# Kernel optimization log

Measured on AMD Instinct MI355X. Metric: run time of the kernel, lower is better.

The kernel has to match this reference:

```python
import jax, jax.numpy as jnp
import numpy as np

H = 8        # num_heads
D = 64       # qkv_dim
E = 512      # embed_dim = H*D
MS = 16      # ms_hidden_dim


def setup_inputs() -> dict:
    key = jax.random.key(0)
    ks = jax.random.split(key, 12)
    b, r, c = 4, 512, 512
    row_emb = jax.random.normal(ks[0], (b, r, E), dtype=jnp.float32)
    col_emb = jax.random.normal(ks[1], (b, c, E), dtype=jnp.float32)
    cost_mat = jax.random.uniform(ks[2], (b, r, c), dtype=jnp.float32)
    attn_mask = jax.random.randint(ks[3], (b, H, r, c), 0, 2) > 0
    s = 1.0 / np.sqrt(E)
    Wq = jax.random.uniform(ks[4], (H * D, E), minval=-s, maxval=s)
    Wk = jax.random.uniform(ks[5], (H * D, E), minval=-s, maxval=s)
    Wv = jax.random.uniform(ks[6], (H * D, E), minval=-s, maxval=s)
    Wout = jax.random.uniform(ks[7], (E, E), minval=-s, maxval=s)
    m1 = np.sqrt(0.5)
    m2 = np.sqrt(1.0 / MS)
    Wmix1 = jax.random.uniform(ks[8], (H * MS, 2 * H), minval=-m1, maxval=m1)
    Wmix2 = jax.random.uniform(ks[9], (H, H * MS), minval=-m2, maxval=m2)
    return {"row_emb": row_emb, "col_emb": col_emb, "cost_mat": cost_mat,
            "attn_mask": attn_mask, "Wq": Wq, "Wk": Wk, "Wv": Wv,
            "Wmix1": Wmix1, "Wmix2": Wmix2, "Wout": Wout}


def reference(row_emb, col_emb, cost_mat, attn_mask, Wq, Wk, Wv, Wmix1, Wmix2, Wout):
    b, r, _ = row_emb.shape
    c = col_emb.shape[1]
    norm = 1.0 / jnp.sqrt(jnp.asarray(D, row_emb.dtype))
    # projections -> [b, h, s, d]
    q = (row_emb @ Wq.T).reshape(b, r, H, D).transpose(0, 2, 1, 3)
    k = (col_emb @ Wk.T).reshape(b, c, H, D).transpose(0, 2, 1, 3)
    v = (col_emb @ Wv.T).reshape(b, c, H, D).transpose(0, 2, 1, 3)
    dot = norm * jnp.einsum('bhrd,bhcd->bhrc', q, k)            # [b,h,r,c]
    cost = jnp.broadcast_to(cost_mat[:, None, :, :], dot.shape)  # [b,h,r,c]
    # stack then rearrange 'b h r c s -> b r c (h s)' (h major, s minor)
    two = jnp.stack([dot, cost], axis=-1)                        # [b,h,r,c,2]
    two = two.transpose(0, 2, 3, 1, 4).reshape(b, r, c, 2 * H)
    hid = jax.nn.relu(two @ Wmix1.T)                             # [b,r,c,H*MS]
    ms = hid @ Wmix2.T                                           # [b,r,c,H]
    logits = ms.transpose(0, 3, 1, 2)                            # [b,h,r,c]
    # mask handling: rows that are fully masked become fully unmasked
    all_masked = jnp.all(attn_mask, axis=-1, keepdims=True)
    mask = jnp.where(all_masked, False, attn_mask)
    logits = jnp.where(mask, -jnp.inf, logits)
    weights = jax.nn.softmax(logits, axis=-1)
    out = jnp.einsum('bhrc,bhcd->bhrd', weights, v)              # [b,h,r,d]
    out = out.transpose(0, 2, 1, 3).reshape(b, r, H * D)         # b s (h d)
    return out @ Wout.T
```

## Files before the change

kernel.cpp:

```cpp
#include <hip/hip_runtime.h>
#include <math.h>

typedef __attribute__((ext_vector_type(8))) short bf16x8;
typedef __attribute__((ext_vector_type(4))) float f32x4;
typedef unsigned short ushort_t;

static __device__ inline unsigned short f2bf(float f) {
    union { float f; unsigned u; } v; v.f = f;
    unsigned r = v.u + 0x7fff + ((v.u >> 16) & 1);
    return (unsigned short)(r >> 16);
}

#if defined(__has_builtin)
#  if __has_builtin(__builtin_amdgcn_cvt_pk_bf16_f32)
#    define HAVE_PK_BF16 1
#  endif
#endif

static __device__ inline unsigned pk2bf(float a, float b) {
#ifdef HAVE_PK_BF16
    auto r = __builtin_amdgcn_cvt_pk_bf16_f32(a, b);
    unsigned u; __builtin_memcpy(&u, &r, 4);
    return u;
#else
    return (unsigned)f2bf(a) | ((unsigned)f2bf(b) << 16);
#endif
}

__global__ __launch_bounds__(256) void convert_all(const float* __restrict__ a0,
                                                   const float* __restrict__ a1,
                                                   const float* __restrict__ a2,
                                                   const float* __restrict__ a3,
                                                   const float* __restrict__ a4,
                                                   const float* __restrict__ a5,
                                                   ushort_t* __restrict__ dst) {
    const size_t e = ((size_t)blockIdx.x * 256 + threadIdx.x) * 4;
    const float* src; size_t off;
    if      (e < 1048576) { src = a0; off = 0; }
    else if (e < 2097152) { src = a1; off = 1048576; }
    else if (e < 2359296) { src = a2; off = 2097152; }
    else if (e < 2621440) { src = a3; off = 2359296; }
    else if (e < 2883584) { src = a4; off = 2621440; }
    else                  { src = a5; off = 2883584; }
    const float4 v = *(const float4*)(src + (e - off));
    uint2 o; o.x = pk2bf(v.x, v.y); o.y = pk2bf(v.z, v.w);
    *(uint2*)(dst + e) = o;
}

template<int OM>
__global__ __launch_bounds__(256) void gemm_bt(const ushort_t* __restrict__ A,
                                               const ushort_t* __restrict__ B,
                                               void* __restrict__ C) {
    const int t    = threadIdx.x;
    const int w    = t >> 6;
    const int lane = t & 63;
    const int quad = lane >> 4;
    const int sl   = lane & 15;
    const int m0 = blockIdx.x * 64 + (w >> 1) * 32;
    const int n0 = blockIdx.y * 64 + (w & 1) * 32;

    f32x4 acc[2][2] = {};

    for (int k0 = 0; k0 < 512; k0 += 32) {
        bf16x8 a[2], b[2];
#pragma unroll
        for (int rs = 0; rs < 2; ++rs)
            a[rs] = *(const bf16x8*)(A + (size_t)(m0 + rs * 16 + sl) * 512 + k0 + quad * 8);
#pragma unroll
        for (int cs = 0; cs < 2; ++cs)
            b[cs] = *(const bf16x8*)(B + (size_t)(n0 + cs * 16 + sl) * 512 + k0 + quad * 8);
#pragma unroll
        for (int rs = 0; rs < 2; ++rs)
#pragma unroll
            for (int cs = 0; cs < 2; ++cs)
                acc[rs][cs] = __builtin_amdgcn_mfma_f32_16x16x32_bf16(a[rs], b[cs], acc[rs][cs], 0, 0, 0);
    }

#pragma unroll
    for (int rs = 0; rs < 2; ++rs)
#pragma unroll
        for (int cs = 0; cs < 2; ++cs) {
            const int n = n0 + cs * 16 + sl;
            if (OM == 2) {
                const int mb   = m0 + rs * 16 + quad * 4;
                const int bidx = mb >> 9, c = mb & 511;
                const int h = n >> 6, d = n & 63;
                ushort4 o;
                o.x = f2bf(acc[rs][cs][0]); o.y = f2bf(acc[rs][cs][1]);
                o.z = f2bf(acc[rs][cs][2]); o.w = f2bf(acc[rs][cs][3]);
                *(ushort4*)((ushort_t*)C + (size_t)(((bidx * 8 + h) * 64 + d)) * 512 + c) = o;
            } else {
#pragma unroll
                for (int reg = 0; reg < 4; ++reg) {
                    const int m = m0 + rs * 16 + quad * 4 + reg;
                    if (OM == 0)
                        ((ushort_t*)C)[(size_t)m * 512 + n] = f2bf(acc[rs][cs][reg]);
                    else
                        ((float*)C)[(size_t)m * 512 + n] = acc[rs][cs][reg];
                }
            }
        }
}

__global__ __launch_bounds__(256) void pv_bt(const ushort_t* __restrict__ P,
                                             const ushort_t* __restrict__ Vt,
                                             ushort_t* __restrict__ Aout) {
    const int t    = threadIdx.x;
    const int w    = t >> 6;
    const int lane = t & 63;
    const int quad = lane >> 4;
    const int sl   = lane & 15;
    const int bh = blockIdx.y;
    const int m0 = blockIdx.x * 64 + (w >> 1) * 32;
    const int n0 = (w & 1) * 32;

    const ushort_t* A = P  + (size_t)bh * 512 * 512;
    const ushort_t* B = Vt + (size_t)bh * 64 * 512;
    ushort_t* Cb = Aout + (size_t)(bh >> 3) * 512 * 512 + (bh & 7) * 64;

    f32x4 acc[2][2] = {};

    for (int k0 = 0; k0 < 512; k0 += 32) {
        bf16x8 a[2], b[2];
#pragma unroll
        for (int rs = 0; rs < 2; ++rs)
            a[rs] = *(const bf16x8*)(A + (size_t)(m0 + rs * 16 + sl) * 512 + k0 + quad * 8);
#pragma unroll
        for (int cs = 0; cs < 2; ++cs)
            b[cs] = *(const bf16x8*)(B + (size_t)(n0 + cs * 16 + sl) * 512 + k0 + quad * 8);
#pragma unroll
        for (int rs = 0; rs < 2; ++rs)
#pragma unroll
            for (int cs = 0; cs < 2; ++cs)
                acc[rs][cs] = __builtin_amdgcn_mfma_f32_16x16x32_bf16(a[rs], b[cs], acc[rs][cs], 0, 0, 0);
    }

#pragma unroll
    for (int rs = 0; rs < 2; ++rs)
#pragma unroll
        for (int cs = 0; cs < 2; ++cs) {
            const int n = n0 + cs * 16 + sl;
#pragma unroll
            for (int reg = 0; reg < 4; ++reg) {
                const int m = m0 + rs * 16 + quad * 4 + reg;
                Cb[(size_t)m * 512 + n] = f2bf(acc[rs][cs][reg]);
            }
        }
}

__global__ __launch_bounds__(256) void dot_mlp_v3(const ushort_t* __restrict__ Qb,
                                                  const ushort_t* __restrict__ Kb,
                                                  const float* __restrict__ cost,
                                                  const float* __restrict__ W1,
                                                  const float* __restrict__ W2,
                                                  float* __restrict__ logits) {
    __shared__ ushort_t Xs[1024 * 18];
    __shared__ ushort_t hidS[4 * 16 * 136];
    __shared__ ushort_t W1fs[128 * 16];
    __shared__ ushort_t W2ss[8 * 128];

    const int b  = blockIdx.z;
    const int r0 = blockIdx.y * 32;
    const int c0 = blockIdx.x * 32;
    const int t    = threadIdx.x;
    const int w    = t >> 6;
    const int lane = t & 63;
    const int quad = lane >> 4;
    const int sl   = lane & 15;

    const bf16x8 zf = {0, 0, 0, 0, 0, 0, 0, 0};

    {
        int4 z = {0, 0, 0, 0};
#pragma unroll
        for (int i = 0; i < 9; ++i) ((int4*)Xs)[t + i * 256] = z;
    }
    if (t < 128) {
        float s = 0.f;
#pragma unroll
        for (int h = 0; h < 8; ++h) {
            W1fs[t * 16 + h] = f2bf(W1[t * 16 + 2 * h]);
            s += W1[t * 16 + 2 * h + 1];
        }
        W1fs[t * 16 + 8] = f2bf(s);
#pragma unroll
        for (int k = 9; k < 16; ++k) W1fs[t * 16 + k] = 0;
    }
#pragma unroll
    for (int i = 0; i < 4; ++i) {
        const int idx = t + i * 256;
        W2ss[idx] = f2bf(W2[idx]);
    }
    __syncthreads();

#pragma unroll
    for (int i = 0; i < 4; ++i) {
        const int cell = t + i * 256;
        const int rl = cell >> 5, cl = cell & 31;
        Xs[cell * 18 + 8] = f2bf(cost[((size_t)b * 512 + r0 + rl) * 512 + c0 + cl]);
    }

    f32x4 dacc[2][2][2];
#pragma unroll
    for (int hh = 0; hh < 2; ++hh) {
        const int h = 2 * w + hh;
        bf16x8 af[2][2], bfr[2][2];
#pragma unroll
        for (int rs = 0; rs < 2; ++rs)
#pragma unroll
            for (int ks = 0; ks < 2; ++ks)
                af[rs][ks] = *(const bf16x8*)(Qb +
                    ((size_t)(b * 512 + r0 + rs * 16 + sl) * 512 + h * 64 + ks * 32 + quad * 8));
#pragma unroll
        for (int cs = 0; cs < 2; ++cs)
#pragma unroll
            for (int ks = 0; ks < 2; ++ks)
                bfr[cs][ks] = *(const bf16x8*)(Kb +
                    ((size_t)(b * 512 + c0 + cs * 16 + sl) * 512 + h * 64 + ks * 32 + quad * 8));
#pragma unroll
        for (int rs = 0; rs < 2; ++rs)
#pragma unroll
            for (int cs = 0; cs < 2; ++cs) {
                f32x4 acc = {0.f, 0.f, 0.f, 0.f};
                acc = __builtin_amdgcn_mfma_f32_16x16x32_bf16(af[rs][0], bfr[cs][0], acc, 0, 0, 0);
                acc = __builtin_amdgcn_mfma_f32_16x16x32_bf16(af[rs][1], bfr[cs][1], acc, 0, 0, 0);
                dacc[hh][rs][cs] = acc;
            }
    }
#pragma unroll
    for (int rs = 0; rs < 2; ++rs)
#pragma unroll
        for (int cs = 0; cs < 2; ++cs)
#pragma unroll
            for (int reg = 0; reg < 4; ++reg) {
                const int cell = (rs * 16 + quad * 4 + reg) * 32 + cs * 16 + sl;
                ((unsigned*)Xs)[cell * 9 + w] =
                    pk2bf(dacc[0][rs][cs][reg] * 0.125f, dacc[1][rs][cs][reg] * 0.125f);
            }

    __syncthreads();

    bf16x8 bw1[8];
#pragma unroll
    for (int nt = 0; nt < 8; ++nt)
        bw1[nt] = (quad < 2) ? *(const bf16x8*)&W1fs[(nt * 16 + sl) * 16 + quad * 8] : zf;
    bf16x8 bw2[4];
#pragma unroll
    for (int ks = 0; ks < 4; ++ks)
        bw2[ks] = (sl < 8) ? *(const bf16x8*)&W2ss[sl * 128 + ks * 32 + quad * 8] : zf;

    ushort_t* hidW = hidS + w * (16 * 136);

    for (int mt = 0; mt < 16; ++mt) {
        const int gmt = w * 16 + mt;
        const int cb  = gmt * 16;

        bf16x8 a1 = zf;
        if (quad < 2) {
            const unsigned* xr = (const unsigned*)Xs + (size_t)(cb + sl) * 9 + quad * 4;
            union { unsigned u[4]; bf16x8 v; } tmp;
            tmp.u[0] = xr[0]; tmp.u[1] = xr[1]; tmp.u[2] = xr[2]; tmp.u[3] = xr[3];
            a1 = tmp.v;
        }
        f32x4 hacc[8];
#pragma unroll
        for (int nt = 0; nt < 8; ++nt) {
            f32x4 z = {0.f, 0.f, 0.f, 0.f};
            hacc[nt] = __builtin_amdgcn_mfma_f32_16x16x32_bf16(a1, bw1[nt], z, 0, 0, 0);
        }
#pragma unroll
        for (int nt = 0; nt < 8; ++nt)
#pragma unroll
            for (int rp = 0; rp < 4; rp += 2) {
                const unsigned u = pk2bf(fmaxf(hacc[nt][rp], 0.f), fmaxf(hacc[nt][rp + 1], 0.f));
                hidW[(quad * 4 + rp) * 136 + nt * 16 + sl]     = (ushort_t)u;
                hidW[(quad * 4 + rp + 1) * 136 + nt * 16 + sl] = (ushort_t)(u >> 16);
            }

        f32x4 acc2 = {0.f, 0.f, 0.f, 0.f};
#pragma unroll
        for (int ks = 0; ks < 4; ++ks) {
            const ushort_t* hp = hidW + sl * 136 + ks * 32 + quad * 8;
            union { unsigned u[4]; bf16x8 v; } tu;
            *(uint2*)&tu.u[0] = *(const uint2*)hp;
            *(uint2*)&tu.u[2] = *(const uint2*)(hp + 4);
            acc2 = __builtin_amdgcn_mfma_f32_16x16x32_bf16(tu.v, bw2[ks], acc2, 0, 0, 0);
        }

        if (sl < 8) {
            const int r = r0 + (gmt >> 1);
            const int cbase = c0 + (gmt & 1) * 16 + quad * 4;
            float4 o; o.x = acc2[0]; o.y = acc2[1]; o.z = acc2[2]; o.w = acc2[3];
            *(float4*)&logits[((size_t)(b * 8 + sl) * 512 + r) * 512 + cbase] = o;
        }
    }
}

__global__ __launch_bounds__(256) void softmax_mask(const float* __restrict__ logits,
                                                    const int* __restrict__ mask,
                                                    ushort_t* __restrict__ Pb) {
    const int wave = threadIdx.x / 64;
    const int lane = threadIdx.x % 64;
    const size_t rowIdx = (size_t)blockIdx.x * 4 + wave;
    const float* lp = logits + rowIdx * 512;
    const int* mp = mask + rowIdx * 512;

    float v[8];
    int   m[8];
    int allm = 1;
#pragma unroll
    for (int i = 0; i < 8; ++i) {
        v[i] = lp[lane + i * 64];
        m[i] = mp[lane + i * 64];
        allm &= (m[i] != 0);
    }
    const bool all_masked = (__all(allm) != 0);

    float mx = -__builtin_inff();
#pragma unroll
    for (int i = 0; i < 8; ++i) {
        const bool keep = all_masked || (m[i] == 0);
        if (keep) mx = fmaxf(mx, v[i]);
    }
#pragma unroll
    for (int s = 32; s > 0; s >>= 1) mx = fmaxf(mx, __shfl_xor(mx, s, 64));

    float e[8];
    float sum = 0.f;
#pragma unroll
    for (int i = 0; i < 8; ++i) {
        const bool keep = all_masked || (m[i] == 0);
        e[i] = keep ? __expf(v[i] - mx) : 0.f;
        sum += e[i];
    }
#pragma unroll
    for (int s = 32; s > 0; s >>= 1) sum += __shfl_xor(sum, s, 64);

    const float inv = 1.f / sum;
#pragma unroll
    for (int i = 0; i < 8; ++i)
        Pb[rowIdx * 512 + lane + i * 64] = f2bf(e[i] * inv);
}

extern "C" void kernel_launch(void* const* d_in, const int* in_sizes, int n_in,
                              void* d_out, int out_size, void* d_ws, size_t ws_size,
                              hipStream_t stream) {
    const float* row_emb = (const float*)d_in[0];
    const float* col_emb = (const float*)d_in[1];
    const float* cost    = (const float*)d_in[2];
    const int*   mask    = (const int*)d_in[3];
    const float* Wq      = (const float*)d_in[4];
    const float* Wk      = (const float*)d_in[5];
    const float* Wv      = (const float*)d_in[6];
    const float* Wmix1   = (const float*)d_in[7];
    const float* Wmix2   = (const float*)d_in[8];
    const float* Wout    = (const float*)d_in[9];
    float* out = (float*)d_out;

    char* ws = (char*)d_ws;
    const size_t MB = (size_t)1 << 20;
    ushort_t* convDst = (ushort_t*)ws;
    ushort_t* rowb  = (ushort_t*)(ws);
    ushort_t* colb  = (ushort_t*)(ws + 2 * MB);
    ushort_t* Wqb   = (ushort_t*)(ws + 4 * MB);
    ushort_t* Wkb   = (ushort_t*)(ws + 4 * MB + 512 * 1024);
    ushort_t* Wvb   = (ushort_t*)(ws + 5 * MB);
    ushort_t* Woutb = (ushort_t*)(ws + 5 * MB + 512 * 1024);
    ushort_t* Qb    = (ushort_t*)(ws + 6 * MB);
    ushort_t* Kb    = (ushort_t*)(ws + 8 * MB);
    ushort_t* Vt    = (ushort_t*)(ws + 10 * MB);
    ushort_t* Aoutb = (ushort_t*)(ws + 12 * MB);
    ushort_t* Pb    = (ushort_t*)(ws + 16 * MB);
    float* logitsBuf = (float*)(ws + 40 * MB);

    convert_all<<<3072, 256, 0, stream>>>(row_emb, col_emb, Wq, Wk, Wv, Wout, convDst);

    dim3 g1(32, 8);
    gemm_bt<0><<<g1, 256, 0, stream>>>(rowb, Wqb, Qb);
    gemm_bt<0><<<g1, 256, 0, stream>>>(colb, Wkb, Kb);
    gemm_bt<2><<<g1, 256, 0, stream>>>(colb, Wvb, Vt);

    dim3 g2(16, 16, 4);
    dot_mlp_v3<<<g2, 256, 0, stream>>>(Qb, Kb, cost, Wmix1, Wmix2, logitsBuf);

    softmax_mask<<<4096, 256, 0, stream>>>(logitsBuf, mask, Pb);

    pv_bt<<<dim3(8, 32), 256, 0, stream>>>(Pb, Vt, Aoutb);

    gemm_bt<1><<<g1, 256, 0, stream>>>(Aoutb, Woutb, out);
}
```

Baseline: 194.9 us.

## Batch QKV GEMMs, fuse softmax with PV, widen dot-MLP kernel to 512 threads

The three Q/K/V projection GEMMs become one launch indexed by blockIdx.z. Softmax and the P·V product are fused so the probabilities stay in shared memory and the bf16 P buffer round-trip through global memory is gone. The dot/MLP kernel moves to 512 threads with one head per wave. It also interleaves the hidden-layer MFMAs with the second-layer MFMA in small chunks, which shrinks the shared hidden buffer and drops the separate zero-fill pass. In exchange, the fused PV kernel issues less MFMA work per block, and the new W2 fragment permutation has to line up with the packed hidden layout.

```diff
diff --git a/kernel.cpp b/kernel.cpp
--- a/kernel.cpp
+++ b/kernel.cpp
@@ -47,10 +47,18 @@
     *(uint2*)(dst + e) = o;
 }
 
-template<int OM>
-__global__ __launch_bounds__(256) void gemm_bt(const ushort_t* __restrict__ A,
-                                               const ushort_t* __restrict__ B,
-                                               void* __restrict__ C) {
+__global__ __launch_bounds__(256) void gemm_qkv(const ushort_t* __restrict__ rowb,
+                                                const ushort_t* __restrict__ colb,
+                                                const ushort_t* __restrict__ Wqb,
+                                                const ushort_t* __restrict__ Wkb,
+                                                const ushort_t* __restrict__ Wvb,
+                                                ushort_t* __restrict__ Qb,
+                                                ushort_t* __restrict__ Kb,
+                                                ushort_t* __restrict__ Vt) {
+    const int z = blockIdx.z;
+    const ushort_t* A = (z == 0) ? rowb : colb;
+    const ushort_t* B = (z == 0) ? Wqb : (z == 1) ? Wkb : Wvb;
+
     const int t    = threadIdx.x;
     const int w    = t >> 6;
     const int lane = t & 63;
@@ -81,42 +89,35 @@
 #pragma unroll
         for (int cs = 0; cs < 2; ++cs) {
             const int n = n0 + cs * 16 + sl;
-            if (OM == 2) {
+            if (z == 2) {
                 const int mb   = m0 + rs * 16 + quad * 4;
                 const int bidx = mb >> 9, c = mb & 511;
                 const int h = n >> 6, d = n & 63;
                 ushort4 o;
                 o.x = f2bf(acc[rs][cs][0]); o.y = f2bf(acc[rs][cs][1]);
                 o.z = f2bf(acc[rs][cs][2]); o.w = f2bf(acc[rs][cs][3]);
-                *(ushort4*)((ushort_t*)C + (size_t)(((bidx * 8 + h) * 64 + d)) * 512 + c) = o;
+                *(ushort4*)(Vt + (size_t)(((bidx * 8 + h) * 64 + d)) * 512 + c) = o;
             } else {
+                ushort_t* C = (z == 0) ? Qb : Kb;
 #pragma unroll
                 for (int reg = 0; reg < 4; ++reg) {
                     const int m = m0 + rs * 16 + quad * 4 + reg;
-                    if (OM == 0)
-                        ((ushort_t*)C)[(size_t)m * 512 + n] = f2bf(acc[rs][cs][reg]);
-                    else
-                        ((float*)C)[(size_t)m * 512 + n] = acc[rs][cs][reg];
+                    C[(size_t)m * 512 + n] = f2bf(acc[rs][cs][reg]);
                 }
             }
         }
 }
 
-__global__ __launch_bounds__(256) void pv_bt(const ushort_t* __restrict__ P,
-                                             const ushort_t* __restrict__ Vt,
-                                             ushort_t* __restrict__ Aout) {
+__global__ __launch_bounds__(256) void gemm_out(const ushort_t* __restrict__ A,
+                                                const ushort_t* __restrict__ B,
+                                                float* __restrict__ C) {
     const int t    = threadIdx.x;
     const int w    = t >> 6;
     const int lane = t & 63;
     const int quad = lane >> 4;
     const int sl   = lane & 15;
-    const int bh = blockIdx.y;
     const int m0 = blockIdx.x * 64 + (w >> 1) * 32;
-    const int n0 = (w & 1) * 32;
-
-    const ushort_t* A = P  + (size_t)bh * 512 * 512;
-    const ushort_t* B = Vt + (size_t)bh * 64 * 512;
-    ushort_t* Cb = Aout + (size_t)(bh >> 3) * 512 * 512 + (bh & 7) * 64;
+    const int n0 = blockIdx.y * 64 + (w & 1) * 32;
 
     f32x4 acc[2][2] = {};
 
@@ -143,19 +144,19 @@
 #pragma unroll
             for (int reg = 0; reg < 4; ++reg) {
                 const int m = m0 + rs * 16 + quad * 4 + reg;
-                Cb[(size_t)m * 512 + n] = f2bf(acc[rs][cs][reg]);
+                C[(size_t)m * 512 + n] = acc[rs][cs][reg];
             }
         }
 }
 
-__global__ __launch_bounds__(256) void dot_mlp_v3(const ushort_t* __restrict__ Qb,
+__global__ __launch_bounds__(512) void dot_mlp_v4(const ushort_t* __restrict__ Qb,
                                                   const ushort_t* __restrict__ Kb,
                                                   const float* __restrict__ cost,
                                                   const float* __restrict__ W1,
                                                   const float* __restrict__ W2,
                                                   float* __restrict__ logits) {
     __shared__ ushort_t Xs[1024 * 18];
-    __shared__ ushort_t hidS[4 * 16 * 136];
+    __shared__ ushort_t hidS[8 * 16 * 36];
     __shared__ ushort_t W1fs[128 * 16];
     __shared__ ushort_t W2ss[8 * 128];
 
@@ -170,11 +171,6 @@
 
     const bf16x8 zf = {0, 0, 0, 0, 0, 0, 0, 0};
 
-    {
-        int4 z = {0, 0, 0, 0};
-#pragma unroll
-        for (int i = 0; i < 9; ++i) ((int4*)Xs)[t + i * 256] = z;
-    }
     if (t < 128) {
         float s = 0.f;
 #pragma unroll
@@ -187,23 +183,19 @@
         for (int k = 9; k < 16; ++k) W1fs[t * 16 + k] = 0;
     }
 #pragma unroll
-    for (int i = 0; i < 4; ++i) {
-        const int idx = t + i * 256;
-        W2ss[idx] = f2bf(W2[idx]);
-    }
-    __syncthreads();
-
-#pragma unroll
-    for (int i = 0; i < 4; ++i) {
-        const int cell = t + i * 256;
+    for (int i = 0; i < 2; ++i) W2ss[t + i * 512] = f2bf(W2[t + i * 512]);
+
+#pragma unroll
+    for (int i = 0; i < 2; ++i) {
+        const int cell = t + i * 512;
         const int rl = cell >> 5, cl = cell & 31;
-        Xs[cell * 18 + 8] = f2bf(cost[((size_t)b * 512 + r0 + rl) * 512 + c0 + cl]);
-    }
-
-    f32x4 dacc[2][2][2];
-#pragma unroll
-    for (int hh = 0; hh < 2; ++hh) {
-        const int h = 2 * w + hh;
+        unsigned* base = (unsigned*)(Xs + cell * 18 + 8);
+        base[0] = (unsigned)f2bf(cost[((size_t)b * 512 + r0 + rl) * 512 + c0 + cl]);
+        base[1] = 0; base[2] = 0; base[3] = 0; base[4] = 0;
+    }
+
+    {
+        const int h = w;
         bf16x8 af[2][2], bfr[2][2];
 #pragma unroll
         for (int rs = 0; rs < 2; ++rs)
@@ -224,19 +216,13 @@
                 f32x4 acc = {0.f, 0.f, 0.f, 0.f};
                 acc = __builtin_amdgcn_mfma_f32_16x16x32_bf16(af[rs][0], bfr[cs][0], acc, 0, 0, 0);
                 acc = __builtin_amdgcn_mfma_f32_16x16x32_bf16(af[rs][1], bfr[cs][1], acc, 0, 0, 0);
-                dacc[hh][rs][cs] = acc;
+#pragma unroll
+                for (int reg = 0; reg < 4; ++reg) {
+                    const int cell = (rs * 16 + quad * 4 + reg) * 32 + cs * 16 + sl;
+                    Xs[cell * 18 + h] = f2bf(acc[reg] * 0.125f);
+                }
             }
     }
-#pragma unroll
-    for (int rs = 0; rs < 2; ++rs)
-#pragma unroll
-        for (int cs = 0; cs < 2; ++cs)
-#pragma unroll
-            for (int reg = 0; reg < 4; ++reg) {
-                const int cell = (rs * 16 + quad * 4 + reg) * 32 + cs * 16 + sl;
-                ((unsigned*)Xs)[cell * 9 + w] =
-                    pk2bf(dacc[0][rs][cs][reg] * 0.125f, dacc[1][rs][cs][reg] * 0.125f);
-            }
 
     __syncthreads();
 
@@ -246,13 +232,22 @@
         bw1[nt] = (quad < 2) ? *(const bf16x8*)&W1fs[(nt * 16 + sl) * 16 + quad * 8] : zf;
     bf16x8 bw2[4];
 #pragma unroll
-    for (int ks = 0; ks < 4; ++ks)
-        bw2[ks] = (sl < 8) ? *(const bf16x8*)&W2ss[sl * 128 + ks * 32 + quad * 8] : zf;
-
-    ushort_t* hidW = hidS + w * (16 * 136);
-
-    for (int mt = 0; mt < 16; ++mt) {
-        const int gmt = w * 16 + mt;
+    for (int ks = 0; ks < 4; ++ks) {
+        union { ushort_t s[8]; bf16x8 v; } tu;
+#pragma unroll
+        for (int i = 0; i < 8; ++i) {
+            const int p  = quad * 8 + i;
+            const int jc = (p >> 1) | ((p & 1) << 4);
+            tu.s[i] = (sl < 8) ? W2ss[sl * 128 + ks * 32 + jc] : (ushort_t)0;
+        }
+        bw2[ks] = tu.v;
+    }
+
+    ushort_t* hidW = hidS + w * (16 * 36);
+
+#pragma unroll
+    for (int mt = 0; mt < 8; ++mt) {
+        const int gmt = w * 8 + mt;
         const int cb  = gmt * 16;
 
         bf16x8 a1 = zf;
@@ -262,28 +257,21 @@
             tmp.u[0] = xr[0]; tmp.u[1] = xr[1]; tmp.u[2] = xr[2]; tmp.u[3] = xr[3];
             a1 = tmp.v;
         }
-        f32x4 hacc[8];
-#pragma unroll
-        for (int nt = 0; nt < 8; ++nt) {
+
+        f32x4 acc2 = {0.f, 0.f, 0.f, 0.f};
+#pragma unroll
+        for (int ks = 0; ks < 4; ++ks) {
             f32x4 z = {0.f, 0.f, 0.f, 0.f};
-            hacc[nt] = __builtin_amdgcn_mfma_f32_16x16x32_bf16(a1, bw1[nt], z, 0, 0, 0);
-        }
-#pragma unroll
-        for (int nt = 0; nt < 8; ++nt)
-#pragma unroll
-            for (int rp = 0; rp < 4; rp += 2) {
-                const unsigned u = pk2bf(fmaxf(hacc[nt][rp], 0.f), fmaxf(hacc[nt][rp + 1], 0.f));
-                hidW[(quad * 4 + rp) * 136 + nt * 16 + sl]     = (ushort_t)u;
-                hidW[(quad * 4 + rp + 1) * 136 + nt * 16 + sl] = (ushort_t)(u >> 16);
-            }
-
-        f32x4 acc2 = {0.f, 0.f, 0.f, 0.f};
-#pragma unroll
-        for (int ks = 0; ks < 4; ++ks) {
-            const ushort_t* hp = hidW + sl * 136 + ks * 32 + quad * 8;
-            union { unsigned u[4]; bf16x8 v; } tu;
-            *(uint2*)&tu.u[0] = *(const uint2*)hp;
-            *(uint2*)&tu.u[2] = *(const uint2*)(hp + 4);
+            const f32x4 h0 = __builtin_amdgcn_mfma_f32_16x16x32_bf16(a1, bw1[2 * ks],     z, 0, 0, 0);
+            const f32x4 h1 = __builtin_amdgcn_mfma_f32_16x16x32_bf16(a1, bw1[2 * ks + 1], z, 0, 0, 0);
+#pragma unroll
+            for (int rp = 0; rp < 4; ++rp)
+                ((unsigned*)hidW)[(quad * 4 + rp) * 18 + sl] =
+                    pk2bf(fmaxf(h0[rp], 0.f), fmaxf(h1[rp], 0.f));
+            union { uint2 u2[2]; bf16x8 v; } tu;
+            const ushort_t* hp = hidW + sl * 36 + quad * 8;
+            tu.u2[0] = *(const uint2*)hp;
+            tu.u2[1] = *(const uint2*)(hp + 4);
             acc2 = __builtin_amdgcn_mfma_f32_16x16x32_bf16(tu.v, bw2[ks], acc2, 0, 0, 0);
         }
 
@@ -296,50 +284,93 @@
     }
 }
 
-__global__ __launch_bounds__(256) void softmax_mask(const float* __restrict__ logits,
-                                                    const int* __restrict__ mask,
-                                                    ushort_t* __restrict__ Pb) {
-    const int wave = threadIdx.x / 64;
-    const int lane = threadIdx.x % 64;
-    const size_t rowIdx = (size_t)blockIdx.x * 4 + wave;
-    const float* lp = logits + rowIdx * 512;
-    const int* mp = mask + rowIdx * 512;
-
-    float v[8];
-    int   m[8];
-    int allm = 1;
-#pragma unroll
-    for (int i = 0; i < 8; ++i) {
-        v[i] = lp[lane + i * 64];
-        m[i] = mp[lane + i * 64];
-        allm &= (m[i] != 0);
-    }
-    const bool all_masked = (__all(allm) != 0);
-
-    float mx = -__builtin_inff();
-#pragma unroll
-    for (int i = 0; i < 8; ++i) {
-        const bool keep = all_masked || (m[i] == 0);
-        if (keep) mx = fmaxf(mx, v[i]);
-    }
-#pragma unroll
-    for (int s = 32; s > 0; s >>= 1) mx = fmaxf(mx, __shfl_xor(mx, s, 64));
-
-    float e[8];
-    float sum = 0.f;
-#pragma unroll
-    for (int i = 0; i < 8; ++i) {
-        const bool keep = all_masked || (m[i] == 0);
-        e[i] = keep ? __expf(v[i] - mx) : 0.f;
-        sum += e[i];
-    }
-#pragma unroll
-    for (int s = 32; s > 0; s >>= 1) sum += __shfl_xor(sum, s, 64);
-
-    const float inv = 1.f / sum;
-#pragma unroll
-    for (int i = 0; i < 8; ++i)
-        Pb[rowIdx * 512 + lane + i * 64] = f2bf(e[i] * inv);
+__global__ __launch_bounds__(256) void softmax_pv(const float* __restrict__ logits,
+                                                  const int* __restrict__ mask,
+                                                  const ushort_t* __restrict__ Vt,
+                                                  ushort_t* __restrict__ Aout) {
+    __shared__ ushort_t Ps[32 * 520];
+
+    const int t    = threadIdx.x;
+    const int w    = t >> 6;
+    const int lane = t & 63;
+    const int quad = lane >> 4;
+    const int sl   = lane & 15;
+    const int rt = blockIdx.x;
+    const int bh = blockIdx.y;
+    const int r0 = rt * 32;
+
+#pragma unroll
+    for (int rr = 0; rr < 8; ++rr) {
+        const int row = w * 8 + rr;
+        const float* lp = logits + ((size_t)bh * 512 + r0 + row) * 512;
+        const int*   mp = mask   + ((size_t)bh * 512 + r0 + row) * 512;
+
+        float v[8]; int m[8]; int allm = 1;
+#pragma unroll
+        for (int i = 0; i < 8; ++i) {
+            v[i] = lp[lane + i * 64];
+            m[i] = mp[lane + i * 64];
+            allm &= (m[i] != 0);
+        }
+        const bool all_masked = (__all(allm) != 0);
+
+        float mx = -__builtin_inff();
+#pragma unroll
+        for (int i = 0; i < 8; ++i) {
+            const bool keep = all_masked || (m[i] == 0);
+            if (keep) mx = fmaxf(mx, v[i]);
+        }
+#pragma unroll
+        for (int s = 32; s > 0; s >>= 1) mx = fmaxf(mx, __shfl_xor(mx, s, 64));
+
+        float e[8]; float sum = 0.f;
+#pragma unroll
+        for (int i = 0; i < 8; ++i) {
+            const bool keep = all_masked || (m[i] == 0);
+            e[i] = keep ? __expf(v[i] - mx) : 0.f;
+            sum += e[i];
+        }
+#pragma unroll
+        for (int s = 32; s > 0; s >>= 1) sum += __shfl_xor(sum, s, 64);
+
+        const float inv = 1.f / sum;
+#pragma unroll
+        for (int i = 0; i < 8; ++i)
+            Ps[row * 520 + lane + i * 64] = f2bf(e[i] * inv);
+    }
+
+    __syncthreads();
+
+    const int mt  = w >> 1;
+    const int n0w = (w & 1) * 32;
+    const ushort_t* vb = Vt + (size_t)bh * 64 * 512;
+
+    f32x4 acc[2] = {};
+    for (int ks = 0; ks < 16; ++ks) {
+        union { uint2 u2[2]; bf16x8 v; } ta;
+        const ushort_t* pp = Ps + (size_t)(mt * 16 + sl) * 520 + ks * 32 + quad * 8;
+        ta.u2[0] = *(const uint2*)pp;
+        ta.u2[1] = *(const uint2*)(pp + 4);
+        bf16x8 bv[2];
+#pragma unroll
+        for (int cn = 0; cn < 2; ++cn)
+            bv[cn] = *(const bf16x8*)(vb + (size_t)(n0w + cn * 16 + sl) * 512 + ks * 32 + quad * 8);
+#pragma unroll
+        for (int cn = 0; cn < 2; ++cn)
+            acc[cn] = __builtin_amdgcn_mfma_f32_16x16x32_bf16(ta.v, bv[cn], acc[cn], 0, 0, 0);
+    }
+
+    const int bidx = bh >> 3, h = bh & 7;
+    ushort_t* Cb = Aout + (size_t)bidx * 512 * 512 + h * 64;
+#pragma unroll
+    for (int cn = 0; cn < 2; ++cn) {
+        const int n = n0w + cn * 16 + sl;
+#pragma unroll
+        for (int reg = 0; reg < 4; ++reg) {
+            const int m = r0 + mt * 16 + quad * 4 + reg;
+            Cb[(size_t)m * 512 + n] = f2bf(acc[cn][reg]);
+        }
+    }
 }
 
 extern "C" void kernel_launch(void* const* d_in, const int* in_sizes, int n_in,
@@ -370,22 +401,15 @@
     ushort_t* Kb    = (ushort_t*)(ws + 8 * MB);
     ushort_t* Vt    = (ushort_t*)(ws + 10 * MB);
     ushort_t* Aoutb = (ushort_t*)(ws + 12 * MB);
-    ushort_t* Pb    = (ushort_t*)(ws + 16 * MB);
     float* logitsBuf = (float*)(ws + 40 * MB);
 
     convert_all<<<3072, 256, 0, stream>>>(row_emb, col_emb, Wq, Wk, Wv, Wout, convDst);
 
-    dim3 g1(32, 8);
-    gemm_bt<0><<<g1, 256, 0, stream>>>(rowb, Wqb, Qb);
-    gemm_bt<0><<<g1, 256, 0, stream>>>(colb, Wkb, Kb);
-    gemm_bt<2><<<g1, 256, 0, stream>>>(colb, Wvb, Vt);
-
-    dim3 g2(16, 16, 4);
-    dot_mlp_v3<<<g2, 256, 0, stream>>>(Qb, Kb, cost, Wmix1, Wmix2, logitsBuf);
-
-    softmax_mask<<<4096, 256, 0, stream>>>(logitsBuf, mask, Pb);
-
-    pv_bt<<<dim3(8, 32), 256, 0, stream>>>(Pb, Vt, Aoutb);
-
-    gemm_bt<1><<<g1, 256, 0, stream>>>(Aoutb, Woutb, out);
-}
+    gemm_qkv<<<dim3(32, 8, 3), 256, 0, stream>>>(rowb, colb, Wqb, Wkb, Wvb, Qb, Kb, Vt);
+
+    dot_mlp_v4<<<dim3(16, 16, 4), 512, 0, stream>>>(Qb, Kb, cost, Wmix1, Wmix2, logitsBuf);
+
+    softmax_pv<<<dim3(16, 32), 256, 0, stream>>>(logitsBuf, mask, Vt, Aoutb);
+
+    gemm_out<<<dim3(32, 8), 256, 0, stream>>>(Aoutb, Woutb, out);
+}
```

After: 186.8 us. -4.1%, faster.
